# Kernel optimization log

Hardware: AMD Instinct MI355X
Metric: run time of the kernel (lower is better)

## Reference

```python
import jax, jax.numpy as jnp
import numpy as np

N_NODES = 50000
N_EDGES = 800000
FEAT = 64
HID = 128
N_TYPES = 4
N_REL = 3
N_LAYERS = 2
LN_EPS = 1e-5


def setup_inputs() -> dict:
    key = jax.random.key(0)
    ks = jax.random.split(key, 20)
    inp = {
        "z": jax.random.randint(ks[0], (N_NODES,), 0, 100, dtype=jnp.int32),
        "node_type": jax.random.randint(ks[1], (N_NODES,), 0, N_TYPES, dtype=jnp.int32),
        "edge_index": jax.random.randint(ks[2], (2, N_EDGES), 0, N_NODES, dtype=jnp.int32),
        "edge_type": jax.random.randint(ks[3], (N_EDGES,), 0, N_REL, dtype=jnp.int32),
        # learned parameters
        "z_embed": jax.random.normal(ks[4], (100, FEAT), jnp.float32),
        "enc_w1": jax.random.normal(ks[5], (N_TYPES, FEAT, HID), jnp.float32) * 0.05,
        "enc_b1": jnp.zeros((N_TYPES, HID), jnp.float32),
        "enc_w2": jax.random.normal(ks[6], (N_TYPES, HID, HID), jnp.float32) * 0.05,
        "enc_b2": jnp.zeros((N_TYPES, HID), jnp.float32),
        "lin_w": jax.random.normal(ks[7], (N_LAYERS, HID, HID), jnp.float32) * 0.05,
        "lin_b": jnp.zeros((N_LAYERS, HID), jnp.float32),
        "rel_w": jax.random.normal(ks[8], (N_LAYERS, N_REL, HID, HID), jnp.float32) * 0.05,
        "ln_g": jnp.ones((N_LAYERS, HID), jnp.float32),
        "ln_b": jnp.zeros((N_LAYERS, HID), jnp.float32),
        "reg_w": jax.random.normal(ks[9], (HID, 1), jnp.float32) * 0.05,
        "reg_b": jnp.zeros((1,), jnp.float32),
    }
    return inp


def _layer_norm(x, g, b):
    mu = jnp.mean(x, axis=-1, keepdims=True)
    var = jnp.mean((x - mu) ** 2, axis=-1, keepdims=True)
    return (x - mu) * jax.lax.rsqrt(var + LN_EPS) * g + b


def reference(z, node_type, edge_index, edge_type, z_embed, enc_w1, enc_b1,
              enc_w2, enc_b2, lin_w, lin_b, rel_w, ln_g, ln_b, reg_w, reg_b):
    n = z.shape[0]
    # FeatureBuilder (site_ads=None path): atomic-number embedding lookup
    raw = z_embed[z]  # [N, FEAT]
    # TypeSpecificEncoder: run all 4 type MLPs, select per node by node_type
    h = jax.nn.relu(jnp.einsum('nd,tdh->nth', raw, enc_w1) + enc_b1)  # [N,T,H]
    enc_all = jnp.einsum('nth,tho->nto', h, enc_w2) + enc_b2           # [N,T,H]
    x = jnp.take_along_axis(enc_all, node_type[:, None, None].astype(jnp.int32), axis=1)[:, 0, :]

    src, dst = edge_index[0], edge_index[1]
    deg = jax.ops.segment_sum(jnp.ones((edge_type.shape[0],), x.dtype), dst, num_segments=n)
    deg = jnp.clip(deg, 1.0, None)[:, None]  # [N,1]

    for l in range(N_LAYERS):
        out = jnp.zeros_like(x)
        x_src = x[src]  # [E, H] gathered source features
        for r in range(N_REL):
            mask = (edge_type == r).astype(x.dtype)[:, None]
            msg = (x_src * mask) @ rel_w[l, r]  # [E, H]
            out = out + jax.ops.segment_sum(msg, dst, num_segments=n)
        out = out / deg
        x = _layer_norm(x @ lin_w[l] + lin_b[l] + out, ln_g[l], ln_b[l])

    pooled = jnp.mean(x, axis=0)  # mean pooling, mask = all ones
    return pooled @ reg_w + reg_b  # [1]
```

## Files before the change

kernel.cpp:

```cpp
#include <hip/hip_runtime.h>

#define N_NODES 50000
#define N_EDGES 800000
#define FEAT 64
#define HID 128
#define N_TYPES 4
#define N_REL 3
#define N_LAYERS 2
#define LN_EPS 1e-5f
#define NROWS 50016
#define NG32 1563
#define CAP 64
#define NBKT 196
#define CAP1 4608
#define EPB 4096
#define BINCAP 56
#define NCOMBO 400
#define WT_STRIDE 136

typedef __attribute__((ext_vector_type(8))) short bf16x8;
typedef __attribute__((ext_vector_type(16))) float f32x16;
typedef __attribute__((ext_vector_type(2))) float f32x2;

static __device__ inline unsigned short f2bf(float f) {
    unsigned int u = __float_as_uint(f);
    return (unsigned short)((u + 0x7fffu + ((u >> 16) & 1u)) >> 16);
}
static __device__ inline unsigned int packbf2(float lo, float hi) {
    return (unsigned int)f2bf(lo) | ((unsigned int)f2bf(hi) << 16);
}

static __device__ inline void acc8_fp8(float* a, uint2 w) {
    f32x2 d0 = __builtin_amdgcn_cvt_pk_f32_fp8((int)w.x, false);
    f32x2 d1 = __builtin_amdgcn_cvt_pk_f32_fp8((int)w.x, true);
    f32x2 d2 = __builtin_amdgcn_cvt_pk_f32_fp8((int)w.y, false);
    f32x2 d3 = __builtin_amdgcn_cvt_pk_f32_fp8((int)w.y, true);
    a[0] += d0[0]; a[1] += d0[1]; a[2] += d1[0]; a[3] += d1[1];
    a[4] += d2[0]; a[5] += d2[1]; a[6] += d3[0]; a[7] += d3[1];
}

__global__ __launch_bounds__(256) void bin1_kernel(const int* __restrict__ src,
                                                   const int* __restrict__ dst,
                                                   const int* __restrict__ et,
                                                   const int* __restrict__ z,
                                                   const int* __restrict__ nt,
                                                   unsigned short* __restrict__ combo,
                                                   int* __restrict__ bcnt,
                                                   int* __restrict__ bucket) {
    int ci = blockIdx.x * 256 + threadIdx.x;
    if (ci < N_NODES) combo[ci] = (unsigned short)(z[ci] * 4 + nt[ci]);

    __shared__ int lbin[NBKT * BINCAP];
    __shared__ int lcnt[NBKT];
    __shared__ int lbase[NBKT];
    for (int i = threadIdx.x; i < NBKT; i += 256) lcnt[i] = 0;
    __syncthreads();
    int base = blockIdx.x * EPB;
#pragma unroll
    for (int i = 0; i < EPB / 256; ++i) {
        int e = base + i * 256 + threadIdx.x;
        if (e < N_EDGES) {
            int d = dst[e];
            int b = d >> 8;
            int v = src[e] | (et[e] << 16) | ((d & 255) << 18);
            int pos = atomicAdd(&lcnt[b], 1);
            if (pos < BINCAP) lbin[b * BINCAP + pos] = v;
        }
    }
    __syncthreads();
    if (threadIdx.x < NBKT) {
        int c = min(lcnt[threadIdx.x], BINCAP);
        lcnt[threadIdx.x] = c;
        lbase[threadIdx.x] = atomicAdd(&bcnt[threadIdx.x], c);
    }
    __syncthreads();
    int wv = threadIdx.x >> 6, ln = threadIdx.x & 63;
    for (int b = wv; b < NBKT; b += 4) {
        int c = lcnt[b];
        if (ln < c) {
            int gp = lbase[b] + ln;
            if (gp < CAP1) bucket[b * CAP1 + gp] = lbin[b * BINCAP + ln];
        }
    }
}

__global__ __launch_bounds__(256) void build2_kernel(const int* __restrict__ bcnt,
                                                     const int* __restrict__ bucket,
                                                     const unsigned short* __restrict__ combo,
                                                     int* __restrict__ cnt3,
                                                     int* __restrict__ payload) {
    __shared__ int lcnt[256 * 3];
    for (int i = threadIdx.x; i < 768; i += 256) lcnt[i] = 0;
    __syncthreads();
    int b = blockIdx.x;
    int n0 = b << 8;
    int cb = min(bcnt[b], CAP1);
    const int* bk = bucket + b * CAP1;
    for (int i = threadIdx.x; i < cb; i += 256) {
        int v = bk[i];
        atomicAdd(&lcnt[((v >> 18) & 255) * 3 + ((v >> 16) & 3)], 1);
    }
    __syncthreads();
    int t = threadIdx.x;
    int c0 = min(lcnt[t * 3 + 0], CAP);
    int c1 = min(lcnt[t * 3 + 1], CAP - c0);
    int c2 = min(lcnt[t * 3 + 2], CAP - c0 - c1);
    __syncthreads();
    lcnt[t * 3 + 0] = 0;
    lcnt[t * 3 + 1] = c0;
    lcnt[t * 3 + 2] = c0 + c1;
    int node = n0 + t;
    if (node < N_NODES) cnt3[node] = c0 | (c1 << 8) | (c2 << 16);
    __syncthreads();
    for (int i = threadIdx.x; i < cb; i += 256) {
        int v = bk[i];
        int dl = (v >> 18) & 255;
        int r = (v >> 16) & 3;
        int sc = v & 0xffff;
        int pos = atomicAdd(&lcnt[dl * 3 + r], 1);
        if (pos < CAP)
            payload[((n0 + dl) << 6) + pos] = sc | ((int)combo[sc] << 18);
    }
}

__global__ __launch_bounds__(128) void table_kernel(const float* __restrict__ z_embed,
                                                    const float* __restrict__ w1,
                                                    const float* __restrict__ b1,
                                                    const float* __restrict__ w2,
                                                    const float* __restrict__ b2,
                                                    const float* __restrict__ rel_w,
                                                    const float* __restrict__ lin_w,
                                                    const float* __restrict__ lin_b,
                                                    unsigned int* __restrict__ ytab,
                                                    float* __restrict__ lintab,
                                                    unsigned short* __restrict__ wbuf,
                                                    float* __restrict__ pooled) {
    if (blockIdx.x >= NCOMBO) {
        int pb = blockIdx.x - NCOMBO;
        if (pb == 0) pooled[threadIdx.x] = 0.0f;
        int idx = pb * 128 + threadIdx.x;
        int k = idx & 127;
        int col = (idx >> 7) & 127;
        int mat = idx >> 14;
        float w = (mat < 3) ? rel_w[(((size_t)(3 + mat)) * HID + k) * HID + col]
                            : lin_w[((size_t)(HID + k)) * HID + col];
        wbuf[(size_t)mat * HID * WT_STRIDE + col * WT_STRIDE + k] = f2bf(w);
        return;
    }
    int c = blockIdx.x;
    int zi = c >> 2;
    int t = c & 3;
    int j = threadIdx.x;
    __shared__ float h[HID];
    __shared__ float xrow[HID];
    __shared__ float tmp[HID];
    float acc = b1[t * HID + j];
#pragma unroll 8
    for (int k = 0; k < FEAT; ++k)
        acc = fmaf(z_embed[zi * FEAT + k], w1[((size_t)t * FEAT + k) * HID + j], acc);
    h[j] = fmaxf(acc, 0.0f);
    __syncthreads();
    float acc2 = b2[t * HID + j];
#pragma unroll 8
    for (int k = 0; k < HID; ++k)
        acc2 = fmaf(h[k], w2[(size_t)t * HID * HID + k * HID + j], acc2);
    xrow[j] = acc2;
    __syncthreads();
#pragma unroll 1
    for (int r = 0; r < N_REL; ++r) {
        float a = 0.f;
        const float* W = rel_w + (size_t)r * HID * HID;
#pragma unroll 8
        for (int k = 0; k < HID; ++k) a = fmaf(xrow[k], W[k * HID + j], a);
        tmp[j] = a;
        __syncthreads();
        if (j < 32) {
            int w0 = __builtin_amdgcn_cvt_pk_fp8_f32(tmp[4 * j], tmp[4 * j + 1], 0, false);
            w0 = __builtin_amdgcn_cvt_pk_fp8_f32(tmp[4 * j + 2], tmp[4 * j + 3], w0, true);
            ytab[(r * NCOMBO + c) * 32 + j] = (unsigned)w0;
        }
        __syncthreads();
    }
    float a = lin_b[j];
#pragma unroll 8
    for (int k = 0; k < HID; ++k) a = fmaf(xrow[k], lin_w[k * HID + j], a);
    lintab[c * HID + j] = a;
}

__global__ __launch_bounds__(256) void gather_ln1_kernel(
    const int* __restrict__ cnt3, const int* __restrict__ payload,
    const uint2* __restrict__ ytab8, const float* __restrict__ lintab,
    const unsigned short* __restrict__ combo, const float* __restrict__ lng,
    const float* __restrict__ lnb, uint4* __restrict__ xb4,
    uint2* __restrict__ xf8) {
    int tid = blockIdx.x * 256 + threadIdx.x;
    int node = tid >> 4;
    int l16 = tid & 15;
    int c3 = cnt3[node];
    int c0 = c3 & 255, c1 = (c3 >> 8) & 255, c2 = (c3 >> 16) & 255;
    int tot = c0 + c1 + c2;
    float inv = 1.0f / (float)max(tot, 1);
    const int* pl = payload + (node << 6);
    float a[8] = {};
    int e = 0;
#pragma unroll 1
    for (int r = 0; r < 3; ++r) {
        int e1 = (r == 0) ? c0 : (r == 1) ? c0 + c1 : tot;
        int base = (r * NCOMBO) << 4;
        for (; e + 2 <= e1; e += 2) {
            int pA = pl[e], pB = pl[e + 1];
            uint2 vA = ytab8[base + ((pA >> 18) << 4) + l16];
            uint2 vB = ytab8[base + ((pB >> 18) << 4) + l16];
            acc8_fp8(a, vA);
            acc8_fp8(a, vB);
        }
        if (e < e1) {
            int p = pl[e]; ++e;
            acc8_fp8(a, ytab8[base + ((p >> 18) << 4) + l16]);
        }
    }
    const float* lrow = lintab + (int)combo[node] * HID + l16 * 8;
    float v[8], s = 0.f, q = 0.f;
#pragma unroll
    for (int j = 0; j < 8; ++j) {
        v[j] = fmaf(a[j], inv, lrow[j]);
        s += v[j];
        q += v[j] * v[j];
    }
#pragma unroll
    for (int mk = 1; mk < 16; mk <<= 1) {
        s += __shfl_xor(s, mk);
        q += __shfl_xor(q, mk);
    }
    float mu = s * (1.0f / HID);
    float rstd = rsqrtf(q * (1.0f / HID) - mu * mu + LN_EPS);
    const float* g8 = lng + l16 * 8;
    const float* b8 = lnb + l16 * 8;
    float o[8];
#pragma unroll
    for (int j = 0; j < 8; ++j) o[j] = (v[j] - mu) * rstd * g8[j] + b8[j];
    uint4 w;
    w.x = packbf2(o[0], o[1]);
    w.y = packbf2(o[2], o[3]);
    w.z = packbf2(o[4], o[5]);
    w.w = packbf2(o[6], o[7]);
    xb4[(node << 4) + l16] = w;
    int lo = 0, hi = 0;
    lo = __builtin_amdgcn_cvt_pk_fp8_f32(o[0], o[1], lo, false);
    lo = __builtin_amdgcn_cvt_pk_fp8_f32(o[2], o[3], lo, true);
    hi = __builtin_amdgcn_cvt_pk_fp8_f32(o[4], o[5], hi, false);
    hi = __builtin_amdgcn_cvt_pk_fp8_f32(o[6], o[7], hi, true);
    xf8[(node << 4) + l16] = make_uint2((unsigned)lo, (unsigned)hi);
}

__global__ __launch_bounds__(256) void gather3_kernel(const int* __restrict__ cnt3,
                                                      const int* __restrict__ payload,
                                                      const uint2* __restrict__ xf8,
                                                      uint4* __restrict__ s0,
                                                      uint4* __restrict__ s1,
                                                      uint4* __restrict__ s2) {
    int tid = blockIdx.x * 256 + threadIdx.x;
    int node = tid >> 4;
    int l16 = tid & 15;
    int c3 = cnt3[node];
    int c0 = c3 & 255, c1 = (c3 >> 8) & 255, c2 = (c3 >> 16) & 255;
    int tot = c0 + c1 + c2;
    float inv = 1.0f / (float)max(tot, 1);
    const int* pl = payload + (node << 6);
    int o = node * 16 + l16;
    int e = 0;
#pragma unroll 1
    for (int r = 0; r < 3; ++r) {
        int e1 = (r == 0) ? c0 : (r == 1) ? c0 + c1 : tot;
        float a[8] = {};
        for (; e + 2 <= e1; e += 2) {
            int pA = pl[e], pB = pl[e + 1];
            uint2 vA = xf8[((pA & 0xffff) << 4) + l16];
            uint2 vB = xf8[((pB & 0xffff) << 4) + l16];
            acc8_fp8(a, vA);
            acc8_fp8(a, vB);
        }
        if (e < e1) {
            int p = pl[e]; ++e;
            acc8_fp8(a, xf8[((p & 0xffff) << 4) + l16]);
        }
        uint4 w;
        w.x = packbf2(a[0] * inv, a[1] * inv);
        w.y = packbf2(a[2] * inv, a[3] * inv);
        w.z = packbf2(a[4] * inv, a[5] * inv);
        w.w = packbf2(a[6] * inv, a[7] * inv);
        if (r == 0) s0[o] = w;
        else if (r == 1) s1[o] = w;
        else s2[o] = w;
    }
}

__global__ __launch_bounds__(512) void fused_layer_kernel(
    const unsigned short* __restrict__ s0, const unsigned short* __restrict__ s1,
    const unsigned short* __restrict__ s2, const unsigned short* __restrict__ xb,
    const uint4* __restrict__ wbuf, const float* __restrict__ lb,
    const float* __restrict__ lng, const float* __restrict__ lnb,
    float* __restrict__ pooled) {
    __shared__ __align__(16) unsigned short Wt[4 * HID * WT_STRIDE];
    __shared__ float csh[3 * HID];
    __shared__ float pooled_sh[HID];

    if (threadIdx.x < HID) {
        pooled_sh[threadIdx.x] = 0.0f;
        csh[threadIdx.x] = lb[threadIdx.x];
        csh[HID + threadIdx.x] = lng[threadIdx.x];
        csh[2 * HID + threadIdx.x] = lnb[threadIdx.x];
    }
    uint4* wt4 = (uint4*)Wt;
#pragma unroll
    for (int i = 0; i < 17; ++i)
        wt4[i * 512 + threadIdx.x] = wbuf[i * 512 + threadIdx.x];
    __syncthreads();

    int wave = threadIdx.x >> 6;
    int lane = threadIdx.x & 63;
    int n32 = lane & 31;
    int hf = lane >> 5;

    float pacc[4] = {0.f, 0.f, 0.f, 0.f};

    for (int g = wave * gridDim.x + blockIdx.x; g < NG32; g += gridDim.x * 8) {
        int node0 = g * 32;
        f32x16 acc[4];
#pragma unroll
        for (int ct = 0; ct < 4; ++ct)
#pragma unroll
            for (int i = 0; i < 16; ++i) acc[ct][i] = 0.0f;

#pragma unroll 1
        for (int mat = 0; mat < 4; ++mat) {
            const unsigned short* asrc = (mat == 0) ? s0 : (mat == 1) ? s1
                                       : (mat == 2) ? s2 : xb;
            const unsigned short* arow = asrc + (size_t)(node0 + n32) * HID + hf * 8;
            const unsigned short* wm = Wt + mat * (HID * WT_STRIDE) + n32 * WT_STRIDE + hf * 8;
#pragma unroll 2
            for (int t = 0; t < 8; ++t) {
                bf16x8 a = *(const bf16x8*)(arow + t * 16);
#pragma unroll
                for (int ct = 0; ct < 4; ++ct) {
                    bf16x8 b = *(const bf16x8*)(wm + ct * 32 * WT_STRIDE + t * 16);
                    acc[ct] = __builtin_amdgcn_mfma_f32_32x32x16_bf16(a, b, acc[ct], 0, 0, 0);
                }
            }
        }
#pragma unroll
        for (int reg = 0; reg < 16; ++reg) {
            int row = node0 + (reg & 3) + 8 * (reg >> 2) + 4 * hf;
            float v[4];
            float s = 0.f, q = 0.f;
#pragma unroll
            for (int ct = 0; ct < 4; ++ct) {
                v[ct] = acc[ct][reg] + csh[ct * 32 + n32];
                s += v[ct];
                q += v[ct] * v[ct];
            }
#pragma unroll
            for (int mk = 1; mk < 32; mk <<= 1) {
                s += __shfl_xor(s, mk);
                q += __shfl_xor(q, mk);
            }
            float mu = s * (1.0f / HID);
            float rstd = rsqrtf(q * (1.0f / HID) - mu * mu + LN_EPS);
            if (row < N_NODES) {
#pragma unroll
                for (int ct = 0; ct < 4; ++ct) {
                    int col = ct * 32 + n32;
                    pacc[ct] += (v[ct] - mu) * rstd * csh[HID + col] + csh[2 * HID + col];
                }
            }
        }
    }

#pragma unroll
    for (int ct = 0; ct < 4; ++ct) {
        float t = pacc[ct] + __shfl_xor(pacc[ct], 32);
        if (hf == 0) atomicAdd(&pooled_sh[ct * 32 + n32], t);
    }
    __syncthreads();
    if (threadIdx.x < HID) atomicAdd(&pooled[threadIdx.x], pooled_sh[threadIdx.x]);
}

__global__ void final_kernel(const float* __restrict__ pooled, const float* __restrict__ reg_w,
                             const float* __restrict__ reg_b, float* __restrict__ out) {
    int lane = threadIdx.x;
    float s = pooled[lane] * reg_w[lane] + pooled[64 + lane] * reg_w[64 + lane];
#pragma unroll
    for (int o = 32; o; o >>= 1) s += __shfl_down(s, o);
    if (lane == 0) out[0] = s * (1.0f / N_NODES) + reg_b[0];
}

extern "C" void kernel_launch(void* const* d_in, const int* in_sizes, int n_in,
                              void* d_out, int out_size, void* d_ws, size_t ws_size,
                              hipStream_t stream) {
    const int* z = (const int*)d_in[0];
    const int* nt = (const int*)d_in[1];
    const int* ei = (const int*)d_in[2];
    const int* et = (const int*)d_in[3];
    const float* z_embed = (const float*)d_in[4];
    const float* enc_w1 = (const float*)d_in[5];
    const float* enc_b1 = (const float*)d_in[6];
    const float* enc_w2 = (const float*)d_in[7];
    const float* enc_b2 = (const float*)d_in[8];
    const float* lin_w = (const float*)d_in[9];
    const float* lin_b = (const float*)d_in[10];
    const float* rel_w = (const float*)d_in[11];
    const float* ln_g = (const float*)d_in[12];
    const float* ln_b = (const float*)d_in[13];
    const float* reg_w = (const float*)d_in[14];
    const float* reg_b = (const float*)d_in[15];
    float* out = (float*)d_out;

    const size_t NHb = (size_t)NROWS * HID;
    char* p = (char*)d_ws;
    unsigned short* xb = (unsigned short*)p;    p += NHb * 2;
    unsigned short* s0 = (unsigned short*)p;    p += NHb * 2;
    unsigned short* s1 = (unsigned short*)p;    p += NHb * 2;
    unsigned short* s2 = (unsigned short*)p;    p += NHb * 2;
    uint2* xf8 = (uint2*)p;                     p += NHb;
    unsigned short* wbuf = (unsigned short*)p;  p += (size_t)4 * HID * WT_STRIDE * 2;
    unsigned int* ytab = (unsigned int*)p;      p += (size_t)N_REL * NCOMBO * HID;
    float* lintab = (float*)p;                  p += NCOMBO * HID * 4;
    unsigned short* combo = (unsigned short*)p; p += N_NODES * 2;
    float* pooled = (float*)p;                  p += HID * 4;
    int* cnt3 = (int*)p;                        p += N_NODES * 4;
    int* bcnt = (int*)p;                        p += NBKT * 4;
    int* bucket = (int*)p;                      p += (size_t)NBKT * CAP1 * 4;
    int* payload = (int*)p;                     p += (size_t)N_NODES * CAP * 4;

    const int* src = ei;
    const int* dst = ei + N_EDGES;

    hipMemsetAsync(bcnt, 0, NBKT * sizeof(int), stream);
    bin1_kernel<<<NBKT, 256, 0, stream>>>(src, dst, et, z, nt, combo, bcnt, bucket);
    build2_kernel<<<NBKT, 256, 0, stream>>>(bcnt, bucket, combo, cnt3, payload);

    table_kernel<<<NCOMBO + 512, 128, 0, stream>>>(z_embed, enc_w1, enc_b1, enc_w2, enc_b2,
                                                   rel_w, lin_w, lin_b, ytab, lintab,
                                                   wbuf, pooled);

    gather_ln1_kernel<<<3125, 256, 0, stream>>>(cnt3, payload, (const uint2*)ytab, lintab,
                                                combo, ln_g, ln_b, (uint4*)xb, xf8);
    gather3_kernel<<<3125, 256, 0, stream>>>(cnt3, payload, xf8,
                                             (uint4*)s0, (uint4*)s1, (uint4*)s2);
    fused_layer_kernel<<<256, 512, 0, stream>>>(
        s0, s1, s2, xb, (const uint4*)wbuf, lin_b + HID, ln_g + HID, ln_b + HID, pooled);

    final_kernel<<<1, 64, 0, stream>>>(pooled, reg_w, reg_b, out);
}
```

Measured before the change: 233.5 us.

## Fuse layer-2 neighbor gather into MFMA layer kernel and fold final reduction

Removes the separate gather3 kernel and its s0/s1/s2 bf16 intermediates. Each lane now gathers fp8 neighbor rows for its node straight into registers, normalises them, packs them to bf16 and feeds MFMA directly. The final regression kernel is folded in through a last-block-done atomic counter. This saves intermediate global writes and reads and two launches, at the cost of 64 float accumulators per lane (register pressure under launch_bounds(512,2)). The gather now runs with one node per 32 lanes instead of 16 lanes per node, which may reduce memory-level parallelism.

```diff
diff --git a/kernel.cpp b/kernel.cpp
--- a/kernel.cpp
+++ b/kernel.cpp
@@ -253,57 +253,18 @@
     xf8[(node << 4) + l16] = make_uint2((unsigned)lo, (unsigned)hi);
 }
 
-__global__ __launch_bounds__(256) void gather3_kernel(const int* __restrict__ cnt3,
-                                                      const int* __restrict__ payload,
-                                                      const uint2* __restrict__ xf8,
-                                                      uint4* __restrict__ s0,
-                                                      uint4* __restrict__ s1,
-                                                      uint4* __restrict__ s2) {
-    int tid = blockIdx.x * 256 + threadIdx.x;
-    int node = tid >> 4;
-    int l16 = tid & 15;
-    int c3 = cnt3[node];
-    int c0 = c3 & 255, c1 = (c3 >> 8) & 255, c2 = (c3 >> 16) & 255;
-    int tot = c0 + c1 + c2;
-    float inv = 1.0f / (float)max(tot, 1);
-    const int* pl = payload + (node << 6);
-    int o = node * 16 + l16;
-    int e = 0;
-#pragma unroll 1
-    for (int r = 0; r < 3; ++r) {
-        int e1 = (r == 0) ? c0 : (r == 1) ? c0 + c1 : tot;
-        float a[8] = {};
-        for (; e + 2 <= e1; e += 2) {
-            int pA = pl[e], pB = pl[e + 1];
-            uint2 vA = xf8[((pA & 0xffff) << 4) + l16];
-            uint2 vB = xf8[((pB & 0xffff) << 4) + l16];
-            acc8_fp8(a, vA);
-            acc8_fp8(a, vB);
-        }
-        if (e < e1) {
-            int p = pl[e]; ++e;
-            acc8_fp8(a, xf8[((p & 0xffff) << 4) + l16]);
-        }
-        uint4 w;
-        w.x = packbf2(a[0] * inv, a[1] * inv);
-        w.y = packbf2(a[2] * inv, a[3] * inv);
-        w.z = packbf2(a[4] * inv, a[5] * inv);
-        w.w = packbf2(a[6] * inv, a[7] * inv);
-        if (r == 0) s0[o] = w;
-        else if (r == 1) s1[o] = w;
-        else s2[o] = w;
-    }
-}
-
-__global__ __launch_bounds__(512) void fused_layer_kernel(
-    const unsigned short* __restrict__ s0, const unsigned short* __restrict__ s1,
-    const unsigned short* __restrict__ s2, const unsigned short* __restrict__ xb,
+__global__ __launch_bounds__(512, 2) void fused_layer_kernel(
+    const int* __restrict__ cnt3, const int* __restrict__ payload,
+    const uint2* __restrict__ xf8, const unsigned short* __restrict__ xb,
     const uint4* __restrict__ wbuf, const float* __restrict__ lb,
     const float* __restrict__ lng, const float* __restrict__ lnb,
-    float* __restrict__ pooled) {
+    float* __restrict__ pooled, const float* __restrict__ reg_w,
+    const float* __restrict__ reg_b, float* __restrict__ out,
+    int* __restrict__ done) {
     __shared__ __align__(16) unsigned short Wt[4 * HID * WT_STRIDE];
     __shared__ float csh[3 * HID];
     __shared__ float pooled_sh[HID];
+    __shared__ int lastFlag;
 
     if (threadIdx.x < HID) {
         pooled_sh[threadIdx.x] = 0.0f;
@@ -326,28 +287,72 @@
 
     for (int g = wave * gridDim.x + blockIdx.x; g < NG32; g += gridDim.x * 8) {
         int node0 = g * 32;
+        int node = node0 + n32;
         f32x16 acc[4];
 #pragma unroll
         for (int ct = 0; ct < 4; ++ct)
 #pragma unroll
             for (int i = 0; i < 16; ++i) acc[ct][i] = 0.0f;
 
+        int c3 = (node < N_NODES) ? cnt3[node] : 0;
+        int c0 = c3 & 255, c1 = (c3 >> 8) & 255, c2 = (c3 >> 16) & 255;
+        int tot = c0 + c1 + c2;
+        float inv = 1.0f / (float)max(tot, 1);
+        const int* pl = payload + (node << 6);
+
+        int e = 0;
 #pragma unroll 1
-        for (int mat = 0; mat < 4; ++mat) {
-            const unsigned short* asrc = (mat == 0) ? s0 : (mat == 1) ? s1
-                                       : (mat == 2) ? s2 : xb;
-            const unsigned short* arow = asrc + (size_t)(node0 + n32) * HID + hf * 8;
-            const unsigned short* wm = Wt + mat * (HID * WT_STRIDE) + n32 * WT_STRIDE + hf * 8;
+        for (int r = 0; r < N_REL; ++r) {
+            int e1 = (r == 0) ? c0 : (r == 1) ? c0 + c1 : tot;
+            float a[64] = {};
+            for (; e + 2 <= e1; e += 2) {
+                int pA = pl[e], pB = pl[e + 1];
+                const uint2* rA = xf8 + (((pA & 0xffff) << 4) + hf);
+                const uint2* rB = xf8 + (((pB & 0xffff) << 4) + hf);
+#pragma unroll
+                for (int t = 0; t < 8; ++t) {
+                    uint2 wA = rA[2 * t];
+                    uint2 wB = rB[2 * t];
+                    acc8_fp8(a + t * 8, wA);
+                    acc8_fp8(a + t * 8, wB);
+                }
+            }
+            if (e < e1) {
+                int p = pl[e]; ++e;
+                const uint2* rA = xf8 + (((p & 0xffff) << 4) + hf);
+#pragma unroll
+                for (int t = 0; t < 8; ++t) acc8_fp8(a + t * 8, rA[2 * t]);
+            }
+            const unsigned short* wm = Wt + r * (HID * WT_STRIDE) + n32 * WT_STRIDE + hf * 8;
+#pragma unroll
+            for (int t = 0; t < 8; ++t) {
+                union { bf16x8 v; unsigned int u[4]; } fa;
+                fa.u[0] = packbf2(a[t * 8 + 0] * inv, a[t * 8 + 1] * inv);
+                fa.u[1] = packbf2(a[t * 8 + 2] * inv, a[t * 8 + 3] * inv);
+                fa.u[2] = packbf2(a[t * 8 + 4] * inv, a[t * 8 + 5] * inv);
+                fa.u[3] = packbf2(a[t * 8 + 6] * inv, a[t * 8 + 7] * inv);
+#pragma unroll
+                for (int ct = 0; ct < 4; ++ct) {
+                    bf16x8 b = *(const bf16x8*)(wm + ct * 32 * WT_STRIDE + t * 16);
+                    acc[ct] = __builtin_amdgcn_mfma_f32_32x32x16_bf16(fa.v, b, acc[ct], 0, 0, 0);
+                }
+            }
+        }
+
+        {
+            const unsigned short* arow = xb + (size_t)(node0 + n32) * HID + hf * 8;
+            const unsigned short* wm = Wt + 3 * (HID * WT_STRIDE) + n32 * WT_STRIDE + hf * 8;
 #pragma unroll 2
             for (int t = 0; t < 8; ++t) {
-                bf16x8 a = *(const bf16x8*)(arow + t * 16);
+                bf16x8 av = *(const bf16x8*)(arow + t * 16);
 #pragma unroll
                 for (int ct = 0; ct < 4; ++ct) {
                     bf16x8 b = *(const bf16x8*)(wm + ct * 32 * WT_STRIDE + t * 16);
-                    acc[ct] = __builtin_amdgcn_mfma_f32_32x32x16_bf16(a, b, acc[ct], 0, 0, 0);
+                    acc[ct] = __builtin_amdgcn_mfma_f32_32x32x16_bf16(av, b, acc[ct], 0, 0, 0);
                 }
             }
         }
+
 #pragma unroll
         for (int reg = 0; reg < 16; ++reg) {
             int row = node0 + (reg & 3) + 8 * (reg >> 2) + 4 * hf;
@@ -383,15 +388,20 @@
     }
     __syncthreads();
     if (threadIdx.x < HID) atomicAdd(&pooled[threadIdx.x], pooled_sh[threadIdx.x]);
-}
-
-__global__ void final_kernel(const float* __restrict__ pooled, const float* __restrict__ reg_w,
-                             const float* __restrict__ reg_b, float* __restrict__ out) {
-    int lane = threadIdx.x;
-    float s = pooled[lane] * reg_w[lane] + pooled[64 + lane] * reg_w[64 + lane];
-#pragma unroll
-    for (int o = 32; o; o >>= 1) s += __shfl_down(s, o);
-    if (lane == 0) out[0] = s * (1.0f / N_NODES) + reg_b[0];
+
+    __threadfence();
+    __syncthreads();
+    if (threadIdx.x == 0)
+        lastFlag = (atomicAdd(done, 1) == (int)gridDim.x - 1);
+    __syncthreads();
+    if (lastFlag && threadIdx.x < 64) {
+        int l = threadIdx.x;
+        float s = atomicAdd(&pooled[l], 0.0f) * reg_w[l] +
+                  atomicAdd(&pooled[64 + l], 0.0f) * reg_w[64 + l];
+#pragma unroll
+        for (int o = 32; o; o >>= 1) s += __shfl_down(s, o);
+        if (l == 0) out[0] = s * (1.0f / N_NODES) + reg_b[0];
+    }
 }
 
 extern "C" void kernel_launch(void* const* d_in, const int* in_sizes, int n_in,
@@ -418,9 +428,6 @@
     const size_t NHb = (size_t)NROWS * HID;
     char* p = (char*)d_ws;
     unsigned short* xb = (unsigned short*)p;    p += NHb * 2;
-    unsigned short* s0 = (unsigned short*)p;    p += NHb * 2;
-    unsigned short* s1 = (unsigned short*)p;    p += NHb * 2;
-    unsigned short* s2 = (unsigned short*)p;    p += NHb * 2;
     uint2* xf8 = (uint2*)p;                     p += NHb;
     unsigned short* wbuf = (unsigned short*)p;  p += (size_t)4 * HID * WT_STRIDE * 2;
     unsigned int* ytab = (unsigned int*)p;      p += (size_t)N_REL * NCOMBO * HID;
@@ -429,13 +436,14 @@
     float* pooled = (float*)p;                  p += HID * 4;
     int* cnt3 = (int*)p;                        p += N_NODES * 4;
     int* bcnt = (int*)p;                        p += NBKT * 4;
+    int* done = (int*)p;                        p += 4;
     int* bucket = (int*)p;                      p += (size_t)NBKT * CAP1 * 4;
     int* payload = (int*)p;                     p += (size_t)N_NODES * CAP * 4;
 
     const int* src = ei;
     const int* dst = ei + N_EDGES;
 
-    hipMemsetAsync(bcnt, 0, NBKT * sizeof(int), stream);
+    hipMemsetAsync(bcnt, 0, (NBKT + 1) * sizeof(int), stream);
     bin1_kernel<<<NBKT, 256, 0, stream>>>(src, dst, et, z, nt, combo, bcnt, bucket);
     build2_kernel<<<NBKT, 256, 0, stream>>>(bcnt, bucket, combo, cnt3, payload);
 
@@ -445,10 +453,7 @@
 
     gather_ln1_kernel<<<3125, 256, 0, stream>>>(cnt3, payload, (const uint2*)ytab, lintab,
                                                 combo, ln_g, ln_b, (uint4*)xb, xf8);
-    gather3_kernel<<<3125, 256, 0, stream>>>(cnt3, payload, xf8,
-                                             (uint4*)s0, (uint4*)s1, (uint4*)s2);
     fused_layer_kernel<<<256, 512, 0, stream>>>(
-        s0, s1, s2, xb, (const uint4*)wbuf, lin_b + HID, ln_g + HID, ln_b + HID, pooled);
-
-    final_kernel<<<1, 64, 0, stream>>>(pooled, reg_w, reg_b, out);
-}
+        cnt3, payload, xf8, xb, (const uint4*)wbuf, lin_b + HID, ln_g + HID, ln_b + HID,
+        pooled, reg_w, reg_b, out, done);
+}
```

Result: slower. 266.1 us (+14.0%).
